# Performance work log

Hardware: AMD Instinct MI355X
Metric: run time of the kernel (lower is better)

## Reference

```python
import jax, jax.numpy as jnp
import numpy as np

N_NODES = 100000
N_EDGES = 1600000
D_FEAT = 128
HIDDEN = 256
N_CLASSES = 40


def setup_inputs() -> dict:
    key = jax.random.key(0)
    ks = jax.random.split(key, 6)
    x = jax.random.normal(ks[0], (N_NODES, D_FEAT), dtype=jnp.float32)
    edge_index = jax.random.randint(ks[1], (2, N_EDGES), 0, N_NODES, dtype=jnp.int32)
    # Glorot-ish scaled weights
    w1_l = jax.random.normal(ks[2], (HIDDEN, D_FEAT), dtype=jnp.float32) / np.sqrt(D_FEAT)
    w1_r = jax.random.normal(ks[3], (HIDDEN, D_FEAT), dtype=jnp.float32) / np.sqrt(D_FEAT)
    w2_l = jax.random.normal(ks[4], (N_CLASSES, HIDDEN), dtype=jnp.float32) / np.sqrt(HIDDEN)
    w2_r = jax.random.normal(ks[5], (N_CLASSES, HIDDEN), dtype=jnp.float32) / np.sqrt(HIDDEN)
    b1_l = jnp.zeros((HIDDEN,), jnp.float32)
    b2_l = jnp.zeros((N_CLASSES,), jnp.float32)
    return {"x": x, "edge_index": edge_index, "w1_l": w1_l, "b1_l": b1_l,
            "w1_r": w1_r, "w2_l": w2_l, "b2_l": b2_l, "w2_r": w2_r}


def _sage_conv(x, src, dst, n_nodes, w_l, b_l, w_r):
    # mean aggregation of source-node features onto target nodes
    msg = x[src]                                                  # [E, d]
    agg = jax.ops.segment_sum(msg, dst, num_segments=n_nodes)     # [N, d]
    cnt = jax.ops.segment_sum(jnp.ones((dst.shape[0], 1), x.dtype), dst,
                              num_segments=n_nodes)               # [N, 1]
    agg = agg / jnp.maximum(cnt, 1.0)
    # out = lin_l(agg) + lin_r(x); lin_l has bias, lin_r does not (PyG default)
    return agg @ w_l.T + b_l + x @ w_r.T


def reference(x, edge_index, w1_l, b1_l, w1_r, w2_l, b2_l, w2_r):
    n_nodes = x.shape[0]
    src, dst = edge_index[0], edge_index[1]
    h = jax.nn.relu(_sage_conv(x, src, dst, n_nodes, w1_l, b1_l, w1_r))
    # dropout is identity in eval mode
    out = _sage_conv(h, src, dst, n_nodes, w2_l, b2_l, w2_r)
    return jax.nn.log_softmax(out, axis=1)
```

## Files before the change

kernel.cpp:

```cpp
#include <hip/hip_runtime.h>
#include <hip/hip_bf16.h>
#include <stdint.h>

#define NN 100000
#define NE 1600000
#define DF 128
#define DH 256
#define NC 40
#define BSHIFT 8
#define NBKT 391
#define EPB 8192
#define NBIN_BLOCKS ((NE + EPB - 1) / EPB)

typedef __attribute__((ext_vector_type(8))) short short8;
typedef __attribute__((ext_vector_type(4))) float f32x4;

typedef const __attribute__((address_space(1))) unsigned int* gas1;
typedef __attribute__((address_space(3))) unsigned int* las3;

__device__ __forceinline__ void gload16(const void* g, void* l) {
  __builtin_amdgcn_global_load_lds((gas1)g, (las3)l, 16, 0, 0);
}

__device__ __forceinline__ unsigned short f2bf(float f) {
  union { float f; unsigned u; } v; v.f = f;
  unsigned r = v.u + 0x7FFFu + ((v.u >> 16) & 1u);
  return (unsigned short)(r >> 16);
}
__device__ __forceinline__ float bflo(unsigned u) {
  union { unsigned u; float f; } v; v.u = u << 16; return v.f;
}
__device__ __forceinline__ float bfhi(unsigned u) {
  union { unsigned u; float f; } v; v.u = u & 0xFFFF0000u; return v.f;
}

__global__ void k_xbf16(const float* __restrict__ x, unsigned* __restrict__ xb) {
  int i = blockIdx.x * blockDim.x + threadIdx.x;
  if (i < NN * 64) {
    float2 v = ((const float2*)x)[i];
    xb[i] = ((unsigned)f2bf(v.y) << 16) | f2bf(v.x);
  }
}

__global__ __launch_bounds__(256) void k_bhist(const int* __restrict__ dst, int* __restrict__ bcnt) {
  __shared__ int h[NBKT];
  int tid = threadIdx.x;
  for (int b = tid; b < NBKT; b += 256) h[b] = 0;
  __syncthreads();
  int base = blockIdx.x * EPB;
  int n = NE - base; if (n > EPB) n = EPB;
  for (int i = tid; i < n; i += 256) atomicAdd(&h[dst[base + i] >> BSHIFT], 1);
  __syncthreads();
  for (int b = tid; b < NBKT; b += 256) if (h[b]) atomicAdd(&bcnt[b], h[b]);
}

__global__ __launch_bounds__(512) void k_bscan(const int* __restrict__ bcnt,
                                               int* __restrict__ boff, int* __restrict__ bcur) {
  __shared__ int s[512];
  int tid = threadIdx.x;
  int v = (tid < NBKT) ? bcnt[tid] : 0;
  s[tid] = v;
  __syncthreads();
  for (int off = 1; off < 512; off <<= 1) {
    int a = (tid >= off) ? s[tid - off] : 0;
    __syncthreads();
    s[tid] += a;
    __syncthreads();
  }
  int excl = s[tid] - v;
  if (tid < NBKT) { boff[tid] = excl; bcur[tid] = excl; }
  if (tid == 0) boff[NBKT] = s[511];
}

__global__ __launch_bounds__(256) void k_bin(const int* __restrict__ src, const int* __restrict__ dst,
                                             int* __restrict__ bcur, unsigned* __restrict__ pairs) {
  __shared__ int hcnt[NBKT];
  __shared__ int hbase[NBKT];
  int tid = threadIdx.x;
  for (int b = tid; b < NBKT; b += 256) hcnt[b] = 0;
  __syncthreads();
  int base = blockIdx.x * EPB;
  int n = NE - base; if (n > EPB) n = EPB;
  for (int i = tid; i < n; i += 256) atomicAdd(&hcnt[dst[base + i] >> BSHIFT], 1);
  __syncthreads();
  for (int b = tid; b < NBKT; b += 256) hbase[b] = hcnt[b] ? atomicAdd(&bcur[b], hcnt[b]) : 0;
  __syncthreads();
  for (int b = tid; b < NBKT; b += 256) hcnt[b] = 0;
  __syncthreads();
  for (int i = tid; i < n; i += 256) {
    int s = src[base + i], d = dst[base + i];
    int b = d >> BSHIFT;
    int slot = atomicAdd(&hcnt[b], 1);
    pairs[hbase[b] + slot] = (unsigned)s | ((unsigned)(d & 255) << 17);
  }
}

__global__ __launch_bounds__(256) void k_csr(const unsigned* __restrict__ pairs,
                                             const int* __restrict__ boff,
                                             int* __restrict__ row_ptr, int* __restrict__ csr) {
  __shared__ int ncnt[256];
  __shared__ int noff[256];
  int tid = threadIdx.x;
  int b = blockIdx.x;
  int base = boff[b], end = boff[b + 1];
  ncnt[tid] = 0;
  __syncthreads();
  for (int e = base + tid; e < end; e += 256) atomicAdd(&ncnt[pairs[e] >> 17], 1);
  __syncthreads();
  int v = ncnt[tid];
  noff[tid] = v;
  __syncthreads();
  for (int off = 1; off < 256; off <<= 1) {
    int a = (tid >= off) ? noff[tid - off] : 0;
    __syncthreads();
    noff[tid] += a;
    __syncthreads();
  }
  int excl = noff[tid] - v;
  __syncthreads();
  noff[tid] = excl;
  ncnt[tid] = 0;
  __syncthreads();
  int gnode = (b << BSHIFT) + tid;
  if (gnode < NN) row_ptr[gnode] = base + excl;
  if (b == NBKT - 1 && tid == 0) row_ptr[NN] = NE;
  for (int e = base + tid; e < end; e += 256) {
    unsigned p = pairs[e];
    int ld = p >> 17;
    int slot = atomicAdd(&ncnt[ld], 1);
    csr[base + noff[ld] + slot] = (int)(p & 0x1FFFFu);
  }
}

__global__ void k_packw(const float* __restrict__ w1l, const float* __restrict__ w1r,
                        const float* __restrict__ w2l, const float* __restrict__ w2r,
                        unsigned short* __restrict__ Wc, unsigned short* __restrict__ W2c) {
  int i = blockIdx.x * blockDim.x + threadIdx.x;
  if (i < 256 * 256) {
    int o = i >> 8, k = i & 255;
    float v = (k < 128) ? w1l[o * 128 + k] : w1r[o * 128 + (k - 128)];
    Wc[i] = f2bf(v);
  }
  int j = i - 256 * 256;
  if (j >= 0 && j < 80 * 256) {
    int o = j >> 8, k = j & 255;
    float v = (o < 40) ? w2l[o * 256 + k] : w2r[(o - 40) * 256 + k];
    W2c[j] = f2bf(v);
  }
}

__global__ void k_agg1(const unsigned* __restrict__ xb, const int* __restrict__ row_ptr,
                       const int* __restrict__ csr_src, unsigned* __restrict__ A1) {
  int w = threadIdx.x >> 6, lane = threadIdx.x & 63;
  int node = blockIdx.x * 4 + w;
  if (node >= NN) return;
  int rs = row_ptr[node], re = row_ptr[node + 1];
  float a0 = 0.f, a1 = 0.f;
  int e = rs;
  for (; e + 7 < re; e += 8) {
    int si[8];
#pragma unroll
    for (int j = 0; j < 8; ++j) si[j] = csr_src[e + j];
    unsigned v[8];
#pragma unroll
    for (int j = 0; j < 8; ++j) v[j] = xb[(size_t)si[j] * 64 + lane];
#pragma unroll
    for (int j = 0; j < 8; ++j) { a0 += bflo(v[j]); a1 += bfhi(v[j]); }
  }
  for (; e < re; ++e) {
    unsigned v0 = xb[(size_t)csr_src[e] * 64 + lane];
    a0 += bflo(v0); a1 += bfhi(v0);
  }
  int deg = re - rs;
  float inv = 1.f / (float)(deg > 0 ? deg : 1);
  unsigned pack = ((unsigned)f2bf(a1 * inv) << 16) | f2bf(a0 * inv);
  A1[(size_t)node * 128 + lane] = pack;
  A1[(size_t)node * 128 + 64 + lane] = xb[(size_t)node * 64 + lane];
}

__global__ __launch_bounds__(256) void k_gemm1(const unsigned short* __restrict__ A1,
                                               const unsigned short* __restrict__ Wc,
                                               const float* __restrict__ b1,
                                               unsigned short* __restrict__ H) {
  __shared__ __align__(16) unsigned short sA[128 * 64];
  __shared__ __align__(16) unsigned short sB[128 * 64];
  int tid = threadIdx.x;
  int w = tid >> 6, lane = tid & 63;
  int brow = blockIdx.x * 128;
  int bcol = blockIdx.y * 128;
  int wr = (w >> 1) * 64, wc = (w & 1) * 64;
  f32x4 acc[4][4] = {};

  for (int kt = 0; kt < 4; ++kt) {
#pragma unroll
    for (int t = 0; t < 4; ++t) {
      int c = (t * 4 + w) * 64 + lane;
      int r = c >> 3, cc = c & 7;
      int scc = cc ^ (r & 7);
      int gr = brow + r; if (gr > NN - 1) gr = NN - 1;
      gload16(A1 + (size_t)gr * 256 + kt * 64 + scc * 8, sA + c * 8);
    }
#pragma unroll
    for (int t = 0; t < 4; ++t) {
      int c = (t * 4 + w) * 64 + lane;
      int r = c >> 3, cc = c & 7;
      int scc = cc ^ (r & 7);
      gload16(Wc + (size_t)(bcol + r) * 256 + kt * 64 + scc * 8, sB + c * 8);
    }
    __syncthreads();
#pragma unroll
    for (int kg = 0; kg < 2; ++kg) {
      short8 af[4], bfr[4];
#pragma unroll
      for (int m = 0; m < 4; ++m) {
        int row = wr + m * 16 + (lane & 15);
        int cch = (kg * 4 + (lane >> 4)) ^ (row & 7);
        af[m] = *(const short8*)(sA + row * 64 + cch * 8);
      }
#pragma unroll
      for (int n = 0; n < 4; ++n) {
        int row = wc + n * 16 + (lane & 15);
        int cch = (kg * 4 + (lane >> 4)) ^ (row & 7);
        bfr[n] = *(const short8*)(sB + row * 64 + cch * 8);
      }
#pragma unroll
      for (int m = 0; m < 4; ++m)
#pragma unroll
        for (int n = 0; n < 4; ++n)
          acc[m][n] = __builtin_amdgcn_mfma_f32_16x16x32_bf16(af[m], bfr[n], acc[m][n], 0, 0, 0);
    }
    __syncthreads();
  }

  int colbase = bcol + wc + (lane & 15);
  int rowbase = brow + wr + (lane >> 4) * 4;
#pragma unroll
  for (int n = 0; n < 4; ++n) {
    int col = colbase + n * 16;
    float bias = b1[col];
#pragma unroll
    for (int m = 0; m < 4; ++m) {
      int row0 = rowbase + m * 16;
#pragma unroll
      for (int q = 0; q < 4; ++q) {
        int row = row0 + q;
        if (row < NN) {
          float v = acc[m][n][q] + bias;
          v = v > 0.f ? v : 0.f;
          H[(size_t)row * 256 + col] = f2bf(v);
        }
      }
    }
  }
}

__global__ __launch_bounds__(256) void k_gemm2(const unsigned short* __restrict__ H,
                                               const unsigned short* __restrict__ W2c,
                                               unsigned short* __restrict__ Pb,
                                               float* __restrict__ R) {
  __shared__ __align__(16) unsigned short sA[128 * 64];
  __shared__ __align__(16) unsigned short sB[80 * 64];
  int tid = threadIdx.x;
  int w = tid >> 6, lane = tid & 63;
  int brow = blockIdx.x * 128;
  f32x4 acc[2][5] = {};

  for (int kt = 0; kt < 4; ++kt) {
#pragma unroll
    for (int t = 0; t < 4; ++t) {
      int c = (t * 4 + w) * 64 + lane;
      int r = c >> 3, cc = c & 7;
      int scc = cc ^ (r & 7);
      int gr = brow + r; if (gr > NN - 1) gr = NN - 1;
      gload16(H + (size_t)gr * 256 + kt * 64 + scc * 8, sA + c * 8);
    }
    for (int g = w; g < 10; g += 4) {
      int c = g * 64 + lane;
      int r = c >> 3, cc = c & 7;
      int scc = cc ^ (r & 7);
      gload16(W2c + (size_t)r * 256 + kt * 64 + scc * 8, sB + c * 8);
    }
    __syncthreads();
#pragma unroll
    for (int kg = 0; kg < 2; ++kg) {
      short8 af[2], bfr[5];
#pragma unroll
      for (int m = 0; m < 2; ++m) {
        int row = w * 32 + m * 16 + (lane & 15);
        int cch = (kg * 4 + (lane >> 4)) ^ (row & 7);
        af[m] = *(const short8*)(sA + row * 64 + cch * 8);
      }
#pragma unroll
      for (int n = 0; n < 5; ++n) {
        int row = n * 16 + (lane & 15);
        int cch = (kg * 4 + (lane >> 4)) ^ (row & 7);
        bfr[n] = *(const short8*)(sB + row * 64 + cch * 8);
      }
#pragma unroll
      for (int m = 0; m < 2; ++m)
#pragma unroll
        for (int n = 0; n < 5; ++n)
          acc[m][n] = __builtin_amdgcn_mfma_f32_16x16x32_bf16(af[m], bfr[n], acc[m][n], 0, 0, 0);
    }
    __syncthreads();
  }

  int colbase = lane & 15;
  int rowbase = brow + w * 32 + (lane >> 4) * 4;
#pragma unroll
  for (int m = 0; m < 2; ++m) {
#pragma unroll
    for (int n = 0; n < 5; ++n) {
      int col = colbase + n * 16;
#pragma unroll
      for (int q = 0; q < 4; ++q) {
        int row = rowbase + m * 16 + q;
        if (row < NN) {
          float v = acc[m][n][q];
          if (col < NC) Pb[(size_t)row * 64 + col] = f2bf(v);
          else {
            R[(size_t)row * NC + (col - NC)] = v;
            if (col < 64) Pb[(size_t)row * 64 + col] = 0;
          }
        }
      }
    }
  }
}

__global__ __launch_bounds__(256) void k_final(const unsigned short* __restrict__ Pb,
                                               const float* __restrict__ R,
                                               const int* __restrict__ row_ptr,
                                               const int* __restrict__ csr_src,
                                               const float* __restrict__ b2,
                                               float* __restrict__ out) {
  int w = threadIdx.x >> 6, lane = threadIdx.x & 63;
  int g = lane >> 4, r = lane & 15;
  int node = blockIdx.x * 4 + w;
  if (node >= NN) return;
  int rs = row_ptr[node], re = row_ptr[node + 1];
  float s0 = 0.f, s1 = 0.f, s2 = 0.f, s3 = 0.f;
  int nfull = (re - rs) >> 3;
  int e = rs + g;
  for (int it = 0; it < nfull; ++it, e += 8) {
    int sa = csr_src[e];
    int sb = csr_src[e + 4];
    uint2 va = *(const uint2*)(Pb + (size_t)sa * 64 + r * 4);
    uint2 vb = *(const uint2*)(Pb + (size_t)sb * 64 + r * 4);
    s0 += bflo(va.x) + bflo(vb.x);
    s1 += bfhi(va.x) + bfhi(vb.x);
    s2 += bflo(va.y) + bflo(vb.y);
    s3 += bfhi(va.y) + bfhi(vb.y);
  }
  if (e < re) {
    int sa = csr_src[e];
    uint2 va = *(const uint2*)(Pb + (size_t)sa * 64 + r * 4);
    s0 += bflo(va.x); s1 += bfhi(va.x); s2 += bflo(va.y); s3 += bfhi(va.y);
  }
  e += 4;
  if (e < re) {
    int sa = csr_src[e];
    uint2 va = *(const uint2*)(Pb + (size_t)sa * 64 + r * 4);
    s0 += bflo(va.x); s1 += bfhi(va.x); s2 += bflo(va.y); s3 += bfhi(va.y);
  }
  s0 += __shfl_xor(s0, 16); s0 += __shfl_xor(s0, 32);
  s1 += __shfl_xor(s1, 16); s1 += __shfl_xor(s1, 32);
  s2 += __shfl_xor(s2, 16); s2 += __shfl_xor(s2, 32);
  s3 += __shfl_xor(s3, 16); s3 += __shfl_xor(s3, 32);

  int deg = re - rs;
  float inv = 1.f / (float)(deg > 0 ? deg : 1);
  bool act = r < 10;
  float4 rr = act ? *(const float4*)(R + (size_t)node * NC + r * 4) : make_float4(0, 0, 0, 0);
  float4 bb = act ? *(const float4*)(b2 + r * 4) : make_float4(0, 0, 0, 0);
  float v0 = s0 * inv + rr.x + bb.x;
  float v1 = s1 * inv + rr.y + bb.y;
  float v2 = s2 * inv + rr.z + bb.z;
  float v3 = s3 * inv + rr.w + bb.w;
  float mx = act ? fmaxf(fmaxf(v0, v1), fmaxf(v2, v3)) : -1e30f;
#pragma unroll
  for (int o = 1; o < 16; o <<= 1) mx = fmaxf(mx, __shfl_xor(mx, o));
  float ex = act ? (__expf(v0 - mx) + __expf(v1 - mx) + __expf(v2 - mx) + __expf(v3 - mx)) : 0.f;
#pragma unroll
  for (int o = 1; o < 16; o <<= 1) ex += __shfl_xor(ex, o);
  float ls = mx + __logf(ex);
  if (g == 0 && act) {
    float4 o4 = make_float4(v0 - ls, v1 - ls, v2 - ls, v3 - ls);
    *(float4*)(out + (size_t)node * NC + r * 4) = o4;
  }
}

extern "C" void kernel_launch(void* const* d_in, const int* in_sizes, int n_in,
                              void* d_out, int out_size, void* d_ws, size_t ws_size,
                              hipStream_t stream) {
  const float* x   = (const float*)d_in[0];
  const int*   ei  = (const int*)d_in[1];
  const float* w1l = (const float*)d_in[2];
  const float* b1  = (const float*)d_in[3];
  const float* w1r = (const float*)d_in[4];
  const float* w2l = (const float*)d_in[5];
  const float* b2  = (const float*)d_in[6];
  const float* w2r = (const float*)d_in[7];
  float* out = (float*)d_out;
  const int* src = ei;
  const int* dst = ei + NE;

  char* ws = (char*)d_ws;
  size_t off = 0;
  auto alloc = [&](size_t bytes) -> char* {
    char* p = ws + off;
    off = (off + bytes + 255) & ~(size_t)255;
    return p;
  };
  int* bcnt     = (int*)alloc((size_t)(NBKT + 1) * 4);
  int* boff     = (int*)alloc((size_t)(NBKT + 1) * 4);
  int* bcur     = (int*)alloc((size_t)NBKT * 4);
  int* row_ptr  = (int*)alloc((size_t)(NN + 1) * 4);
  unsigned* pairs = (unsigned*)alloc((size_t)NE * 4);
  int* csr      = (int*)alloc((size_t)NE * 4);
  unsigned short* Wc  = (unsigned short*)alloc(256 * 256 * 2);
  unsigned short* W2c = (unsigned short*)alloc(80 * 256 * 2);
  unsigned*       xb  = (unsigned*)alloc((size_t)NN * 64 * 4);
  unsigned*       A1  = (unsigned*)alloc((size_t)NN * 128 * 4);
  unsigned short* H   = (unsigned short*)alloc((size_t)NN * 256 * 2);
  unsigned short* Pb  = (unsigned short*)alloc((size_t)NN * 64 * 2);
  float*          R   = (float*)alloc((size_t)NN * NC * 4);

  hipMemsetAsync(bcnt, 0, (size_t)(NBKT + 1) * 4, stream);
  k_bhist<<<NBIN_BLOCKS, 256, 0, stream>>>(dst, bcnt);
  k_xbf16<<<(NN * 64 + 255) / 256, 256, 0, stream>>>(x, xb);
  k_bscan<<<1, 512, 0, stream>>>(bcnt, boff, bcur);
  k_bin<<<NBIN_BLOCKS, 256, 0, stream>>>(src, dst, bcur, pairs);
  k_csr<<<NBKT, 256, 0, stream>>>(pairs, boff, row_ptr, csr);
  k_packw<<<336, 256, 0, stream>>>(w1l, w1r, w2l, w2r, Wc, W2c);
  k_agg1<<<(NN + 3) / 4, 256, 0, stream>>>(xb, row_ptr, csr, A1);
  dim3 g1((NN + 127) / 128, 2);
  k_gemm1<<<g1, 256, 0, stream>>>((const unsigned short*)A1, Wc, b1, H);
  k_gemm2<<<(NN + 127) / 128, 256, 0, stream>>>(H, W2c, Pb, R);
  k_final<<<(NN + 3) / 4, 256, 0, stream>>>(Pb, R, row_ptr, csr, b2, out);
}
```

Baseline: 376.1 us.

## Drop self-feature copy into A1 and widen GEMM1 to full output width

```diff
diff --git a/kernel.cpp b/kernel.cpp
--- a/kernel.cpp
+++ b/kernel.cpp
@@ -156,90 +156,88 @@
   if (node >= NN) return;
   int rs = row_ptr[node], re = row_ptr[node + 1];
   float a0 = 0.f, a1 = 0.f;
-  int e = rs;
-  for (; e + 7 < re; e += 8) {
-    int si[8];
-#pragma unroll
-    for (int j = 0; j < 8; ++j) si[j] = csr_src[e + j];
+  for (int e = rs; e < re; e += 8) {
     unsigned v[8];
 #pragma unroll
-    for (int j = 0; j < 8; ++j) v[j] = xb[(size_t)si[j] * 64 + lane];
+    for (int j = 0; j < 8; ++j) {
+      int ej = e + j;
+      int idx = csr_src[ej < re ? ej : re - 1];
+      unsigned t = xb[(size_t)idx * 64 + lane];
+      v[j] = (ej < re) ? t : 0u;
+    }
 #pragma unroll
     for (int j = 0; j < 8; ++j) { a0 += bflo(v[j]); a1 += bfhi(v[j]); }
-  }
-  for (; e < re; ++e) {
-    unsigned v0 = xb[(size_t)csr_src[e] * 64 + lane];
-    a0 += bflo(v0); a1 += bfhi(v0);
   }
   int deg = re - rs;
   float inv = 1.f / (float)(deg > 0 ? deg : 1);
   unsigned pack = ((unsigned)f2bf(a1 * inv) << 16) | f2bf(a0 * inv);
-  A1[(size_t)node * 128 + lane] = pack;
-  A1[(size_t)node * 128 + 64 + lane] = xb[(size_t)node * 64 + lane];
-}
-
-__global__ __launch_bounds__(256) void k_gemm1(const unsigned short* __restrict__ A1,
+  A1[(size_t)node * 64 + lane] = pack;
+}
+
+__global__ __launch_bounds__(512) void k_gemm1(const unsigned short* __restrict__ A1,
+                                               const unsigned short* __restrict__ XB,
                                                const unsigned short* __restrict__ Wc,
                                                const float* __restrict__ b1,
                                                unsigned short* __restrict__ H) {
   __shared__ __align__(16) unsigned short sA[128 * 64];
-  __shared__ __align__(16) unsigned short sB[128 * 64];
+  __shared__ __align__(16) unsigned short sB[256 * 64];
   int tid = threadIdx.x;
   int w = tid >> 6, lane = tid & 63;
   int brow = blockIdx.x * 128;
-  int bcol = blockIdx.y * 128;
-  int wr = (w >> 1) * 64, wc = (w & 1) * 64;
-  f32x4 acc[4][4] = {};
+  int wr = (w >> 1) * 32, wc = (w & 1) * 128;
+  f32x4 acc[2][8] = {};
 
   for (int kt = 0; kt < 4; ++kt) {
-#pragma unroll
-    for (int t = 0; t < 4; ++t) {
-      int c = (t * 4 + w) * 64 + lane;
+    const unsigned short* srcA = (kt < 2) ? A1 : XB;
+    int kcol = (kt & 1) * 64;
+#pragma unroll
+    for (int t = 0; t < 2; ++t) {
+      int c = t * 512 + tid;
       int r = c >> 3, cc = c & 7;
       int scc = cc ^ (r & 7);
       int gr = brow + r; if (gr > NN - 1) gr = NN - 1;
-      gload16(A1 + (size_t)gr * 256 + kt * 64 + scc * 8, sA + c * 8);
+      gload16(srcA + (size_t)gr * 128 + kcol + scc * 8, sA + c * 8);
     }
 #pragma unroll
     for (int t = 0; t < 4; ++t) {
-      int c = (t * 4 + w) * 64 + lane;
+      int c = t * 512 + tid;
       int r = c >> 3, cc = c & 7;
       int scc = cc ^ (r & 7);
-      gload16(Wc + (size_t)(bcol + r) * 256 + kt * 64 + scc * 8, sB + c * 8);
+      gload16(Wc + (size_t)r * 256 + kt * 64 + scc * 8, sB + c * 8);
     }
     __syncthreads();
 #pragma unroll
     for (int kg = 0; kg < 2; ++kg) {
-      short8 af[4], bfr[4];
-#pragma unroll
-      for (int m = 0; m < 4; ++m) {
+      short8 af[2], bfr[8];
+#pragma unroll
+      for (int m = 0; m < 2; ++m) {
         int row = wr + m * 16 + (lane & 15);
         int cch = (kg * 4 + (lane >> 4)) ^ (row & 7);
         af[m] = *(const short8*)(sA + row * 64 + cch * 8);
       }
 #pragma unroll
-      for (int n = 0; n < 4; ++n) {
+      for (int n = 0; n < 8; ++n) {
         int row = wc + n * 16 + (lane & 15);
         int cch = (kg * 4 + (lane >> 4)) ^ (row & 7);
         bfr[n] = *(const short8*)(sB + row * 64 + cch * 8);
       }
 #pragma unroll
-      for (int m = 0; m < 4; ++m)
-#pragma unroll
-        for (int n = 0; n < 4; ++n)
+      for (int m = 0; m < 2; ++m)
+#pragma unroll
+        for (int n = 0; n < 8; ++n)
           acc[m][n] = __builtin_amdgcn_mfma_f32_16x16x32_bf16(af[m], bfr[n], acc[m][n], 0, 0, 0);
     }
     __syncthreads();
   }
 
-  int colbase = bcol + wc + (lane & 15);
+  int colbase = wc + (lane & 15);
   int rowbase = brow + wr + (lane >> 4) * 4;
 #pragma unroll
-  for (int n = 0; n < 4; ++n) {
+  for (int n = 0; n < 8; ++n) {
     int col = colbase + n * 16;
     float bias = b1[col];
 #pragma unroll
-    for (int m = 0; m < 4; ++m) {
+    for (int m = 0; m < 2; ++m) {
       int row0 = rowbase + m * 16;
 #pragma unroll
       for (int q = 0; q < 4; ++q) {
@@ -421,7 +419,7 @@
   unsigned short* Wc  = (unsigned short*)alloc(256 * 256 * 2);
   unsigned short* W2c = (unsigned short*)alloc(80 * 256 * 2);
   unsigned*       xb  = (unsigned*)alloc((size_t)NN * 64 * 4);
-  unsigned*       A1  = (unsigned*)alloc((size_t)NN * 128 * 4);
+  unsigned*       A1  = (unsigned*)alloc((size_t)NN * 64 * 4);
   unsigned short* H   = (unsigned short*)alloc((size_t)NN * 256 * 2);
   unsigned short* Pb  = (unsigned short*)alloc((size_t)NN * 64 * 2);
   float*          R   = (float*)alloc((size_t)NN * NC * 4);
@@ -434,8 +432,8 @@
   k_csr<<<NBKT, 256, 0, stream>>>(pairs, boff, row_ptr, csr);
   k_packw<<<336, 256, 0, stream>>>(w1l, w1r, w2l, w2r, Wc, W2c);
   k_agg1<<<(NN + 3) / 4, 256, 0, stream>>>(xb, row_ptr, csr, A1);
-  dim3 g1((NN + 127) / 128, 2);
-  k_gemm1<<<g1, 256, 0, stream>>>((const unsigned short*)A1, Wc, b1, H);
+  k_gemm1<<<(NN + 127) / 128, 512, 0, stream>>>((const unsigned short*)A1,
+                                                (const unsigned short*)xb, Wc, b1, H);
   k_gemm2<<<(NN + 127) / 128, 256, 0, stream>>>(H, W2c, Pb, R);
   k_final<<<(NN + 3) / 4, 256, 0, stream>>>(Pb, R, row_ptr, csr, b2, out);
 }
```

Measured after the change: 362.3 us. 3.7% less time.
